# Performance work log

Measured on AMD Instinct MI355X. Metric: run time of the kernel, lower is better.

## Reference

```python
import jax, jax.numpy as jnp
import numpy as np

# Dims: C cells, L gene tokens, E embed, H mlp hidden, M factors, K topk
C, L, E, H, M, K = 16, 8192, 512, 256, 128, 30
TAU = 1.0        # gumbel-softmax temperature
SOFTNESS = 0.01  # soft-mask sharpness
TEMP = 1.0       # logits temperature
EPS = 1e-20


def setup_inputs() -> dict:
    key = jax.random.key(0)
    ks = jax.random.split(key, 7)
    x = jax.random.normal(ks[0], (C, L, E), dtype=jnp.float32)
    key_padding_mask = jax.random.randint(ks[1], (C, L), 0, 2) > 0  # True = valid
    uniform_noise = jax.random.uniform(ks[2], (C, L - 1, M), dtype=jnp.float32)
    W1 = jax.random.normal(ks[3], (E, H), dtype=jnp.float32) * (1.0 / np.sqrt(E))
    b1 = jnp.zeros((H,), dtype=jnp.float32)
    W2 = jax.random.normal(ks[4], (H, M), dtype=jnp.float32) * (1.0 / np.sqrt(H))
    b2 = jnp.zeros((M,), dtype=jnp.float32)
    return {"x": x, "key_padding_mask": key_padding_mask,
            "uniform_noise": uniform_noise,
            "W1": W1, "b1": b1, "W2": W2, "b2": b2}


def reference(x, key_padding_mask, uniform_noise, W1, b1, W2, b2):
    # default gene_subset: drop token 0, keep the rest  -> S = L-1
    xs = x[:, 1:, :]                          # (C, S, E)
    kpm = key_padding_mask[:, 1:]             # (C, S)

    # 2-layer MLP router (dropout p=0 -> identity)
    h = jax.nn.relu(jnp.einsum('cse,eh->csh', xs, W1) + b1)   # (C, S, H)
    logits = (jnp.einsum('csh,hm->csm', h, W2) + b2) / TEMP    # (C, S, M)

    # GumbelTopK, training path: gumbel-softmax then smooth top-k mask
    gumbel = -jnp.log(-jnp.log(uniform_noise + EPS) + EPS)
    perturbed = (logits + gumbel) / TAU
    probs = jax.nn.softmax(perturbed, axis=-1)                 # (C, S, M)
    topk_vals, _ = jax.lax.top_k(probs, K)                     # (C, S, K)
    threshold = topk_vals[..., -1:]                            # (C, S, 1)
    smooth_mask = jax.nn.sigmoid((probs - threshold) / SOFTNESS)
    out = probs * smooth_mask

    # faithful to the source: mask = ~key_padding_mask; probs *= mask
    out = out * (~kpm)[..., None].astype(out.dtype)
    return out, kpm
```

## Files before the change

kernel.cpp:

```cpp
#include <hip/hip_runtime.h>

#define CC 16
#define LL 8192
#define SS 8191
#define EE 512
#define HH 256
#define MM 128
#define TOPK 30

typedef __attribute__((ext_vector_type(8))) short short8;
typedef __attribute__((ext_vector_type(4))) float f32x4;

static __device__ __forceinline__ unsigned short f2bf(float f) {
    unsigned u = __builtin_bit_cast(unsigned, f);
    u += 0x7FFFu + ((u >> 16) & 1u);
    return (unsigned short)(u >> 16);
}

__global__ void prep_weights(const float* __restrict__ W1, const float* __restrict__ W2,
                             unsigned short* __restrict__ W1T, unsigned short* __restrict__ W2T)
{
    const int b = blockIdx.x, tid = threadIdx.x;
    if (b < 64) {
        const int e0 = b * 8, h = tid;
        short8 sv;
#pragma unroll
        for (int j = 0; j < 8; ++j)
            sv[j] = (short)f2bf(W1[(size_t)(e0 + j) * HH + h]);
        *(short8*)(void*)(W1T + (size_t)h * EE + e0) = sv;
    } else {
        const int h0 = (b - 64) * 16;
        if (tid < MM) {
            const int m = tid;
            short8 s0v, s1v;
#pragma unroll
            for (int j = 0; j < 8; ++j) {
                s0v[j] = (short)f2bf(W2[(size_t)(h0 + j) * MM + m]);
                s1v[j] = (short)f2bf(W2[(size_t)(h0 + 8 + j) * MM + m]);
            }
            *(short8*)(void*)(W2T + (size_t)m * HH + h0) = s0v;
            *(short8*)(void*)(W2T + (size_t)m * HH + h0 + 8) = s1v;
        }
    }
}

__global__ __launch_bounds__(256, 5)
void gene_router_kernel(const float* __restrict__ x,
                        const int*   __restrict__ mask,
                        const float* __restrict__ noise,
                        const unsigned short* __restrict__ W1T,
                        const float* __restrict__ b1,
                        const unsigned short* __restrict__ W2T,
                        const float* __restrict__ b2,
                        float* __restrict__ out,
                        float* __restrict__ outk)
{
    __shared__ unsigned char lds[32 * 1024];

    const int tid = threadIdx.x;
    const int c   = blockIdx.y;
    const int s0  = blockIdx.x * 32;

    {
        const float* xb = x + ((size_t)c * LL + s0 + 1) * EE;
#pragma unroll
        for (int it = 0; it < 8; ++it) {
            const int chunk = it * 256 + tid;
            const int row = chunk >> 6, cc = chunk & 63;
            const int half = cc >> 5, slot = cc & 31;
            const int rs = min(s0 + row, SS - 1) - s0;
            const float* p = xb + (size_t)rs * EE + cc * 8;
            const float4 a = *(const float4*)p;
            const float4 b = *(const float4*)(p + 4);
            short8 sv;
            sv[0]=(short)f2bf(a.x); sv[1]=(short)f2bf(a.y); sv[2]=(short)f2bf(a.z); sv[3]=(short)f2bf(a.w);
            sv[4]=(short)f2bf(b.x); sv[5]=(short)f2bf(b.y); sv[6]=(short)f2bf(b.z); sv[7]=(short)f2bf(b.w);
            *(short8*)(void*)(lds + half * 16384 + row * 512 + ((slot * 16) ^ ((row & 7) << 4))) = sv;
        }
    }
    __syncthreads();

    const int w  = tid >> 6;
    const int lane = tid & 63;
    const int lr = lane & 15;
    const int kq = lane >> 4;

    f32x4 acc[2][4];
#pragma unroll
    for (int r = 0; r < 2; ++r)
#pragma unroll
        for (int n = 0; n < 4; ++n) acc[r][n] = (f32x4)0.0f;

    const int cw = w * 64;
#pragma unroll 4
    for (int ks = 0; ks < 16; ++ks) {
        short8 af[2];
#pragma unroll
        for (int r = 0; r < 2; ++r) {
            const int row = r * 16 + lr;
            af[r] = *(const short8*)(const void*)(lds + (ks >> 3) * 16384 + row * 512
                        + ((((ks & 7) * 64) + kq * 16) ^ ((row & 7) << 4)));
        }
        short8 bf[4];
#pragma unroll
        for (int n = 0; n < 4; ++n)
            bf[n] = *(const short8*)(const void*)(W1T + (size_t)(cw + n * 16 + lr) * EE + ks * 32 + kq * 8);
#pragma unroll
        for (int r = 0; r < 2; ++r)
#pragma unroll
            for (int n = 0; n < 4; ++n)
                acc[r][n] = __builtin_amdgcn_mfma_f32_16x16x32_bf16(af[r], bf[n], acc[r][n], 0, 0, 0);
    }
    __syncthreads();

#pragma unroll
    for (int n = 0; n < 4; ++n) {
        const int colh = cw + n * 16 + lr;
        const float bb = b1[colh];
#pragma unroll
        for (int r = 0; r < 2; ++r)
#pragma unroll
            for (int q = 0; q < 4; ++q) {
                const int row = r * 16 + kq * 4 + q;
                const unsigned short hv = f2bf(fmaxf(acc[r][n][q] + bb, 0.0f));
                *(unsigned short*)(lds + row * 512 + ((colh * 2) ^ ((row & 7) << 4))) = hv;
            }
    }
    __syncthreads();

    f32x4 acc2[2][2];
#pragma unroll
    for (int r = 0; r < 2; ++r)
#pragma unroll
        for (int n = 0; n < 2; ++n) acc2[r][n] = (f32x4)0.0f;

    const int cw2 = w * 32;
#pragma unroll 2
    for (int ks = 0; ks < 8; ++ks) {
        short8 ah[2];
#pragma unroll
        for (int r = 0; r < 2; ++r) {
            const int row = r * 16 + lr;
            ah[r] = *(const short8*)(const void*)(lds + row * 512 + ((ks * 64 + kq * 16) ^ ((row & 7) << 4)));
        }
        short8 bw[2];
#pragma unroll
        for (int n = 0; n < 2; ++n)
            bw[n] = *(const short8*)(const void*)(W2T + (size_t)(cw2 + n * 16 + lr) * HH + ks * 32 + kq * 8);
#pragma unroll
        for (int r = 0; r < 2; ++r)
#pragma unroll
            for (int n = 0; n < 2; ++n)
                acc2[r][n] = __builtin_amdgcn_mfma_f32_16x16x32_bf16(ah[r], bw[n], acc2[r][n], 0, 0, 0);
    }

    float* sL = (float*)(lds + 16384);
#pragma unroll
    for (int r = 0; r < 2; ++r)
#pragma unroll
        for (int n = 0; n < 2; ++n)
#pragma unroll
            for (int q = 0; q < 4; ++q) {
                const int row = r * 16 + kq * 4 + q;
                const int col = cw2 + n * 16 + lr;
                sL[row * 128 + col] = acc2[r][n][q];
            }
    __syncthreads();

    const int tx = tid & 15;
    const int ty = tid >> 4;

    float b2v[8];
    {
        const float4 bb0 = *(const float4*)(b2 + tx * 8 + 0);
        const float4 bb1 = *(const float4*)(b2 + tx * 8 + 4);
        b2v[0]=bb0.x; b2v[1]=bb0.y; b2v[2]=bb0.z; b2v[3]=bb0.w;
        b2v[4]=bb1.x; b2v[5]=bb1.y; b2v[6]=bb1.z; b2v[7]=bb1.w;
    }

    float pr[2][8];
    float pmaxv[2];
#pragma unroll
    for (int i = 0; i < 2; ++i) {
        const int row = ty * 2 + i;
        const int s  = s0 + row;
        const int sc = min(s, SS - 1);
        const float* np_ = noise + ((size_t)c * SS + sc) * MM + tx * 8;
        const float4 u0 = *(const float4*)(np_ + 0);
        const float4 u1 = *(const float4*)(np_ + 4);
        const float uu[8] = {u0.x,u0.y,u0.z,u0.w,u1.x,u1.y,u1.z,u1.w};
        float pm[8];
#pragma unroll
        for (int q = 0; q < 8; ++q) {
            const float g = -__logf(-__logf(uu[q] + 1e-20f) + 1e-20f);
            pm[q] = sL[row * 128 + tx * 8 + q] + b2v[q] + g;
        }
        float mx = pm[0];
#pragma unroll
        for (int q = 1; q < 8; ++q) mx = fmaxf(mx, pm[q]);
        for (int d = 1; d < 16; d <<= 1) mx = fmaxf(mx, __shfl_xor(mx, d, 16));
        float se = 0.0f;
#pragma unroll
        for (int q = 0; q < 8; ++q) { pr[i][q] = __expf(pm[q] - mx); se += pr[i][q]; }
        for (int d = 1; d < 16; d <<= 1) se += __shfl_xor(se, d, 16);
        const float inv = 1.0f / se;
#pragma unroll
        for (int q = 0; q < 8; ++q) pr[i][q] *= inv;
        pmaxv[i] = inv;
    }

    float thr_[2];
#pragma unroll
    for (int i = 0; i < 2; ++i) {
        float lo = 0.0f;
        float hi = fminf(pmaxv[i], 1.0f / 30.0f);
        for (int it = 0; it < 24; ++it) {
            const float mid = 0.5f * (lo + hi);
            int cnt = 0;
#pragma unroll
            for (int q = 0; q < 8; ++q) cnt += (pr[i][q] > mid) ? 1 : 0;
            for (int d = 1; d < 16; d <<= 1) cnt += __shfl_xor(cnt, d, 16);
            const bool ge = (cnt >= TOPK);
            lo = ge ? mid : lo;
            hi = ge ? hi : mid;
        }
        int cnt = 0;
#pragma unroll
        for (int q = 0; q < 8; ++q) cnt += (pr[i][q] > hi) ? 1 : 0;
        for (int d = 1; d < 16; d <<= 1) cnt += __shfl_xor(cnt, d, 16);

        int rep = TOPK - cnt;
        float t = hi, T = hi;
        bool leq = true;
        for (int guard = 0; guard < 32 && rep > 0; ++guard) {
            float m = -1.0f;
#pragma unroll
            for (int q = 0; q < 8; ++q) {
                const float v = pr[i][q];
                const bool in = leq ? (v <= t) : (v < t);
                m = fmaxf(m, in ? v : -1.0f);
            }
            for (int d = 1; d < 16; d <<= 1) m = fmaxf(m, __shfl_xor(m, d, 16));
            int ce = 0;
#pragma unroll
            for (int q = 0; q < 8; ++q) ce += (pr[i][q] == m) ? 1 : 0;
            for (int d = 1; d < 16; d <<= 1) ce += __shfl_xor(ce, d, 16);
            T = m;
            if (ce == 0) break;
            rep -= ce;
            t = m;
            leq = false;
        }
        thr_[i] = T;
    }

#pragma unroll
    for (int i = 0; i < 2; ++i) {
        const int s = s0 + ty * 2 + i;
        if (s < SS) {
            const float mz = (mask[(size_t)c * LL + s + 1] != 0) ? 0.0f : 1.0f;
            float ov[8];
#pragma unroll
            for (int q = 0; q < 8; ++q) {
                const float sm = 1.0f / (1.0f + __expf((thr_[i] - pr[i][q]) * 100.0f));
                ov[q] = pr[i][q] * sm * mz;
            }
            float* op = out + ((size_t)c * SS + s) * MM + tx * 8;
            float4 o0, o1;
            o0.x=ov[0]; o0.y=ov[1]; o0.z=ov[2]; o0.w=ov[3];
            o1.x=ov[4]; o1.y=ov[5]; o1.z=ov[6]; o1.w=ov[7];
            *(float4*)(op + 0) = o0;
            *(float4*)(op + 4) = o1;
        }
    }

    if (tid < 32) {
        const int s = s0 + tid;
        if (s < SS)
            outk[(size_t)c * SS + s] = (mask[(size_t)c * LL + s + 1] != 0) ? 1.0f : 0.0f;
    }
}

extern "C" void kernel_launch(void* const* d_in, const int* in_sizes, int n_in,
                              void* d_out, int out_size, void* d_ws, size_t ws_size,
                              hipStream_t stream) {
    const float* x     = (const float*)d_in[0];
    const int*   mask  = (const int*)d_in[1];
    const float* noise = (const float*)d_in[2];
    const float* W1    = (const float*)d_in[3];
    const float* b1    = (const float*)d_in[4];
    const float* W2    = (const float*)d_in[5];
    const float* b2    = (const float*)d_in[6];
    float* out  = (float*)d_out;
    float* outk = out + (size_t)CC * SS * MM;

    unsigned short* W1T = (unsigned short*)d_ws;
    unsigned short* W2T = W1T + (size_t)HH * EE;

    prep_weights<<<dim3(80), dim3(256), 0, stream>>>(W1, W2, W1T, W2T);

    dim3 grid(256, CC);
    gene_router_kernel<<<grid, dim3(256), 0, stream>>>(x, mask, noise, W1T, b1, W2T, b2, out, outk);
}
```

Measured before the change: 217.7 us.

## Load x straight into MFMA fragments and fuse two-row top-k bisection

The kernel no longer stages the bf16-converted x tile in shared memory. Each lane loads its fp32 A-fragment directly from global memory inside the K loop and converts it with packed bf16 intrinsics. This drops one barrier and lets LDS shrink to a padded logits buffer, so the occupancy hint goes from 5 to 6 blocks. The top-k threshold search now bisects both rows at once using a packed count, runs fewer iterations, and drops the exact tie-resolution pass. That makes the threshold a close approximation of the k-th value, and the direct global loads give up the coalesced staging pattern.

```diff
diff --git a/kernel.cpp b/kernel.cpp
--- a/kernel.cpp
+++ b/kernel.cpp
@@ -1,4 +1,5 @@
 #include <hip/hip_runtime.h>
+#include <hip/hip_bf16.h>
 
 #define CC 16
 #define LL 8192
@@ -10,11 +11,28 @@
 
 typedef __attribute__((ext_vector_type(8))) short short8;
 typedef __attribute__((ext_vector_type(4))) float f32x4;
+typedef __attribute__((ext_vector_type(4))) unsigned int u32x4;
 
 static __device__ __forceinline__ unsigned short f2bf(float f) {
     unsigned u = __builtin_bit_cast(unsigned, f);
     u += 0x7FFFu + ((u >> 16) & 1u);
     return (unsigned short)(u >> 16);
+}
+
+static __device__ __forceinline__ unsigned pk2(float lo, float hi) {
+    __hip_bfloat162 t = __float22bfloat162_rn(float2{lo, hi});
+    unsigned u;
+    __builtin_memcpy(&u, &t, 4);
+    return u;
+}
+
+static __device__ __forceinline__ short8 cvt8(const float4 a, const float4 b) {
+    u32x4 uv;
+    uv[0] = pk2(a.x, a.y);
+    uv[1] = pk2(a.z, a.w);
+    uv[2] = pk2(b.x, b.y);
+    uv[3] = pk2(b.z, b.w);
+    return __builtin_bit_cast(short8, uv);
 }
 
 __global__ void prep_weights(const float* __restrict__ W1, const float* __restrict__ W2,
@@ -44,7 +62,7 @@
     }
 }
 
-__global__ __launch_bounds__(256, 5)
+__global__ __launch_bounds__(256, 6)
 void gene_router_kernel(const float* __restrict__ x,
                         const int*   __restrict__ mask,
                         const float* __restrict__ noise,
@@ -55,35 +73,17 @@
                         float* __restrict__ out,
                         float* __restrict__ outk)
 {
-    __shared__ unsigned char lds[32 * 1024];
+    __shared__ float sLf[32 * 132];
+    unsigned char* ldsb = (unsigned char*)sLf;
 
     const int tid = threadIdx.x;
     const int c   = blockIdx.y;
     const int s0  = blockIdx.x * 32;
 
-    {
-        const float* xb = x + ((size_t)c * LL + s0 + 1) * EE;
-#pragma unroll
-        for (int it = 0; it < 8; ++it) {
-            const int chunk = it * 256 + tid;
-            const int row = chunk >> 6, cc = chunk & 63;
-            const int half = cc >> 5, slot = cc & 31;
-            const int rs = min(s0 + row, SS - 1) - s0;
-            const float* p = xb + (size_t)rs * EE + cc * 8;
-            const float4 a = *(const float4*)p;
-            const float4 b = *(const float4*)(p + 4);
-            short8 sv;
-            sv[0]=(short)f2bf(a.x); sv[1]=(short)f2bf(a.y); sv[2]=(short)f2bf(a.z); sv[3]=(short)f2bf(a.w);
-            sv[4]=(short)f2bf(b.x); sv[5]=(short)f2bf(b.y); sv[6]=(short)f2bf(b.z); sv[7]=(short)f2bf(b.w);
-            *(short8*)(void*)(lds + half * 16384 + row * 512 + ((slot * 16) ^ ((row & 7) << 4))) = sv;
-        }
-    }
-    __syncthreads();
-
-    const int w  = tid >> 6;
+    const int w    = tid >> 6;
     const int lane = tid & 63;
-    const int lr = lane & 15;
-    const int kq = lane >> 4;
+    const int lr   = lane & 15;
+    const int kq   = lane >> 4;
 
     f32x4 acc[2][4];
 #pragma unroll
@@ -91,27 +91,34 @@
 #pragma unroll
         for (int n = 0; n < 4; ++n) acc[r][n] = (f32x4)0.0f;
 
+    const float* xbase = x + ((size_t)c * LL + s0 + 1) * EE + kq * 8;
+    const float* aptr[2];
+#pragma unroll
+    for (int r = 0; r < 2; ++r) {
+        const int rloc = min(s0 + r * 16 + lr, SS - 1) - s0;
+        aptr[r] = xbase + (size_t)rloc * EE;
+    }
+
     const int cw = w * 64;
-#pragma unroll 4
+#pragma unroll 2
     for (int ks = 0; ks < 16; ++ks) {
         short8 af[2];
 #pragma unroll
         for (int r = 0; r < 2; ++r) {
-            const int row = r * 16 + lr;
-            af[r] = *(const short8*)(const void*)(lds + (ks >> 3) * 16384 + row * 512
-                        + ((((ks & 7) * 64) + kq * 16) ^ ((row & 7) << 4)));
-        }
-        short8 bf[4];
+            const float4 a0 = *(const float4*)(aptr[r] + ks * 32);
+            const float4 a1 = *(const float4*)(aptr[r] + ks * 32 + 4);
+            af[r] = cvt8(a0, a1);
+        }
+        short8 bf_[4];
 #pragma unroll
         for (int n = 0; n < 4; ++n)
-            bf[n] = *(const short8*)(const void*)(W1T + (size_t)(cw + n * 16 + lr) * EE + ks * 32 + kq * 8);
+            bf_[n] = *(const short8*)(const void*)(W1T + (size_t)(cw + n * 16 + lr) * EE + ks * 32 + kq * 8);
 #pragma unroll
         for (int r = 0; r < 2; ++r)
 #pragma unroll
             for (int n = 0; n < 4; ++n)
-                acc[r][n] = __builtin_amdgcn_mfma_f32_16x16x32_bf16(af[r], bf[n], acc[r][n], 0, 0, 0);
-    }
-    __syncthreads();
+                acc[r][n] = __builtin_amdgcn_mfma_f32_16x16x32_bf16(af[r], bf_[n], acc[r][n], 0, 0, 0);
+    }
 
 #pragma unroll
     for (int n = 0; n < 4; ++n) {
@@ -123,7 +130,7 @@
             for (int q = 0; q < 4; ++q) {
                 const int row = r * 16 + kq * 4 + q;
                 const unsigned short hv = f2bf(fmaxf(acc[r][n][q] + bb, 0.0f));
-                *(unsigned short*)(lds + row * 512 + ((colh * 2) ^ ((row & 7) << 4))) = hv;
+                *(unsigned short*)(ldsb + row * 512 + ((colh * 2) ^ ((row & 7) << 4))) = hv;
             }
     }
     __syncthreads();
@@ -141,7 +148,7 @@
 #pragma unroll
         for (int r = 0; r < 2; ++r) {
             const int row = r * 16 + lr;
-            ah[r] = *(const short8*)(const void*)(lds + row * 512 + ((ks * 64 + kq * 16) ^ ((row & 7) << 4)));
+            ah[r] = *(const short8*)(const void*)(ldsb + row * 512 + ((ks * 64 + kq * 16) ^ ((row & 7) << 4)));
         }
         short8 bw[2];
 #pragma unroll
@@ -153,8 +160,8 @@
             for (int n = 0; n < 2; ++n)
                 acc2[r][n] = __builtin_amdgcn_mfma_f32_16x16x32_bf16(ah[r], bw[n], acc2[r][n], 0, 0, 0);
     }
-
-    float* sL = (float*)(lds + 16384);
+    __syncthreads();
+
 #pragma unroll
     for (int r = 0; r < 2; ++r)
 #pragma unroll
@@ -163,7 +170,7 @@
             for (int q = 0; q < 4; ++q) {
                 const int row = r * 16 + kq * 4 + q;
                 const int col = cw2 + n * 16 + lr;
-                sL[row * 128 + col] = acc2[r][n][q];
+                sLf[row * 132 + col] = acc2[r][n][q];
             }
     __syncthreads();
 
@@ -193,7 +200,7 @@
 #pragma unroll
         for (int q = 0; q < 8; ++q) {
             const float g = -__logf(-__logf(uu[q] + 1e-20f) + 1e-20f);
-            pm[q] = sL[row * 128 + tx * 8 + q] + b2v[q] + g;
+            pm[q] = sLf[row * 132 + tx * 8 + q] + b2v[q] + g;
         }
         float mx = pm[0];
 #pragma unroll
@@ -209,50 +216,25 @@
         pmaxv[i] = inv;
     }
 
-    float thr_[2];
-#pragma unroll
-    for (int i = 0; i < 2; ++i) {
-        float lo = 0.0f;
-        float hi = fminf(pmaxv[i], 1.0f / 30.0f);
-        for (int it = 0; it < 24; ++it) {
-            const float mid = 0.5f * (lo + hi);
-            int cnt = 0;
-#pragma unroll
-            for (int q = 0; q < 8; ++q) cnt += (pr[i][q] > mid) ? 1 : 0;
-            for (int d = 1; d < 16; d <<= 1) cnt += __shfl_xor(cnt, d, 16);
-            const bool ge = (cnt >= TOPK);
-            lo = ge ? mid : lo;
-            hi = ge ? hi : mid;
-        }
+    float lo0 = 0.0f, lo1 = 0.0f;
+    float hi0 = fminf(pmaxv[0], 1.0f / 30.0f);
+    float hi1 = fminf(pmaxv[1], 1.0f / 30.0f);
+    for (int it = 0; it < 20; ++it) {
+        const float mid0 = 0.5f * (lo0 + hi0);
+        const float mid1 = 0.5f * (lo1 + hi1);
         int cnt = 0;
 #pragma unroll
-        for (int q = 0; q < 8; ++q) cnt += (pr[i][q] > hi) ? 1 : 0;
+        for (int q = 0; q < 8; ++q) {
+            cnt += (pr[0][q] > mid0) ? 1 : 0;
+            cnt += (pr[1][q] > mid1) ? 256 : 0;
+        }
         for (int d = 1; d < 16; d <<= 1) cnt += __shfl_xor(cnt, d, 16);
-
-        int rep = TOPK - cnt;
-        float t = hi, T = hi;
-        bool leq = true;
-        for (int guard = 0; guard < 32 && rep > 0; ++guard) {
-            float m = -1.0f;
-#pragma unroll
-            for (int q = 0; q < 8; ++q) {
-                const float v = pr[i][q];
-                const bool in = leq ? (v <= t) : (v < t);
-                m = fmaxf(m, in ? v : -1.0f);
-            }
-            for (int d = 1; d < 16; d <<= 1) m = fmaxf(m, __shfl_xor(m, d, 16));
-            int ce = 0;
-#pragma unroll
-            for (int q = 0; q < 8; ++q) ce += (pr[i][q] == m) ? 1 : 0;
-            for (int d = 1; d < 16; d <<= 1) ce += __shfl_xor(ce, d, 16);
-            T = m;
-            if (ce == 0) break;
-            rep -= ce;
-            t = m;
-            leq = false;
-        }
-        thr_[i] = T;
-    }
+        const bool ge0 = (cnt & 255) >= TOPK;
+        const bool ge1 = (cnt >> 8)  >= TOPK;
+        lo0 = ge0 ? mid0 : lo0;  hi0 = ge0 ? hi0 : mid0;
+        lo1 = ge1 ? mid1 : lo1;  hi1 = ge1 ? hi1 : mid1;
+    }
+    const float thr_[2] = {hi0, hi1};
 
 #pragma unroll
     for (int i = 0; i < 2; ++i) {
```

After: 298.5 us. +37.1%, slower.
